# Kernel optimization log

Hardware: AMD Instinct MI355X
Metric: run time of the kernel (lower is better)

The kernel has to match this reference:

```python
import jax, jax.numpy as jnp
import numpy as np

B, N, VF, EF, DV, DE, LN = 64, 64, 32, 16, 128, 128, 4
EPS_INNER = 128.0  # BatchNorm1d(MAX_N, internal_d_vert): 2nd positional arg is eps (faithful to source bug)
EPS_BN = 1e-5


def gev_layer(v_in, e_in, evW, evb, eW, eb, vW, vb, relu=True):
    act = jax.nn.relu if relu else (lambda x: x)
    ev = v_in @ evW + evb                                   # [B,N,De]
    # outer_v_sum: ev.unsqueeze(1) + ev.unsqueeze(2) -> [B,N,N,De]
    e_out = act(e_in @ eW + eb + ev[:, None, :, :] + ev[:, :, None, :])
    per_v_e = e_out.sum(axis=1)                             # sum-aggregate over dim 1
    v_out = act(jnp.concatenate([per_v_e, v_in], axis=-1) @ vW + vb)
    return v_out, e_out


def bn_flat(v, g, b):
    # BatchNorm1d(N*VF) on [B, N*VF] in training mode (biased var)
    x = v.reshape(-1, N * VF)
    mu = x.mean(axis=0)
    var = x.var(axis=0)
    x = (x - mu) * jax.lax.rsqrt(var + EPS_BN) * g + b
    return x.reshape(-1, N, VF)


def bn_inner(v, g, b):
    # BatchNorm1d(MAX_N, eps=128) on [B, N, D]: channels are the N axis, stats over (B, D)
    mu = v.mean(axis=(0, 2), keepdims=True)
    var = v.var(axis=(0, 2), keepdims=True)
    return (v - mu) * jax.lax.rsqrt(var + EPS_INNER) * g[None, :, None] + b[None, :, None]


def setup_inputs() -> dict:
    key = jax.random.key(0)
    ks = jax.random.split(key, 24)
    s = 0.01  # force_lin_init with init_noise=0.01, biases zero
    nrm = lambda k, shp: jax.random.normal(k, shp, dtype=jnp.float32) * s
    inp = {
        "v": jax.random.normal(ks[0], (B, N, VF), dtype=jnp.float32),
        "e": jax.random.normal(ks[1], (B, N, N, EF), dtype=jnp.float32),
        "bn_in_g": jnp.ones((N * VF,), jnp.float32),
        "bn_in_b": jnp.zeros((N * VF,), jnp.float32),
        "g1_evW": nrm(ks[2], (VF, DE)), "g1_evb": jnp.zeros((DE,), jnp.float32),
        "g1_eW": nrm(ks[3], (EF, DE)), "g1_eb": jnp.zeros((DE,), jnp.float32),
        "g1_vW": nrm(ks[4], (VF + DE, DV)), "g1_vb": jnp.zeros((DV,), jnp.float32),
        "inn_evW": nrm(ks[5], (LN, DV, DE)), "inn_evb": jnp.zeros((LN, DE), jnp.float32),
        "inn_eW": nrm(ks[6], (LN, DE, DE)), "inn_eb": jnp.zeros((LN, DE), jnp.float32),
        "inn_vW": nrm(ks[7], (LN, DV + DE, DV)), "inn_vb": jnp.zeros((LN, DV), jnp.float32),
        "bn_g": jnp.ones((LN, N), jnp.float32),
        "bn_b": jnp.zeros((LN, N), jnp.float32),
        "g3_evW": nrm(ks[8], (DV, 1)), "g3_evb": jnp.zeros((1,), jnp.float32),
        "g3_eW": nrm(ks[9], (DE, 1)), "g3_eb": jnp.zeros((1,), jnp.float32),
        "g3_vW": nrm(ks[10], (DV + 1, 1)), "g3_vb": jnp.zeros((1,), jnp.float32),
    }
    return inp


def reference(v, e, bn_in_g, bn_in_b, g1_evW, g1_evb, g1_eW, g1_eb, g1_vW, g1_vb,
              inn_evW, inn_evb, inn_eW, inn_eb, inn_vW, inn_vb, bn_g, bn_b,
              g3_evW, g3_evb, g3_eW, g3_eb, g3_vW, g3_vb):
    v = bn_flat(v, bn_in_g, bn_in_b)
    v, e = gev_layer(v, e, g1_evW, g1_evb, g1_eW, g1_eb, g1_vW, g1_vb)
    for i in range(LN):
        v_next, e_next = gev_layer(v, e, inn_evW[i], inn_evb[i], inn_eW[i], inn_eb[i], inn_vW[i], inn_vb[i])
        v = v_next + v  # resnet
        e = e_next + e
        v = bn_inner(v, bn_g[i], bn_b[i])
    v, e = gev_layer(v, e, g3_evW, g3_evb, g3_eW, g3_eb, g3_vW, g3_vb, relu=False)
    return v, e
```

## Files before the change

### kernel.cpp

```cpp
#include <hip/hip_runtime.h>
#include <hip/hip_bf16.h>


typedef __bf16 bf16_t;
typedef __bf16 bf16x8 __attribute__((ext_vector_type(8)));
typedef __bf16 bf16x4 __attribute__((ext_vector_type(4)));
typedef float f32x4 __attribute__((ext_vector_type(4)));

__device__ __forceinline__ void bar_lgkm() {
  asm volatile("s_waitcnt lgkmcnt(0)\n\ts_barrier" ::: "memory");
}

__device__ __forceinline__ unsigned pack2(float a, float b) {
  bf16_t ba = (bf16_t)a, bb = (bf16_t)b;
  unsigned short ua, ub;
  __builtin_memcpy(&ua, &ba, 2);
  __builtin_memcpy(&ub, &bb, 2);
  return (unsigned)ua | ((unsigned)ub << 16);
}
__device__ __forceinline__ float blo(unsigned u) {
  unsigned v = u << 16; float f; __builtin_memcpy(&f, &v, 4); return f;
}
__device__ __forceinline__ float bhi(unsigned u) {
  unsigned v = u & 0xffff0000u; float f; __builtin_memcpy(&f, &v, 4); return f;
}

__global__ __launch_bounds__(256) void k_prep(const float* __restrict__ vin,
    const float* __restrict__ g, const float* __restrict__ bt,
    const float* __restrict__ eW, const float* __restrict__ inn_vW,
    const float* __restrict__ g1_vW, const float* __restrict__ inn_evW,
    float* __restrict__ v0, bf16_t* __restrict__ Wt, float* __restrict__ stats,
    unsigned* __restrict__ vWp, unsigned* __restrict__ g1_vWp,
    unsigned* __restrict__ evWp) {
  const int blk = blockIdx.x, tid = threadIdx.x;
  if (blk < 8) {
    int ch = blk * 256 + tid;
    float s = 0.f, s2 = 0.f;
    for (int b = 0; b < 64; ++b) { float x = vin[b * 2048 + ch]; s += x; s2 += x * x; }
    float mu = s * (1.f / 64.f);
    float var = s2 * (1.f / 64.f) - mu * mu;
    float sc = rsqrtf(var + 1e-5f) * g[ch];
    float bb = bt[ch];
    for (int b = 0; b < 64; ++b) {
      float x = vin[b * 2048 + ch];
      v0[b * 2048 + ch] = (x - mu) * sc + bb;
    }
  } else if (blk < 264) {
    int idx = (blk - 8) * 256 + tid;
    int l = idx >> 14, r = idx & 16383, n = r >> 7, k = r & 127;
    Wt[idx] = (bf16_t)eW[(l << 14) + (k << 7) + n];
  } else if (blk == 264) {
    for (int i = tid; i < 512; i += 256) stats[i] = 0.f;
  } else if (blk < 521) {
    int idx = (blk - 265) * 256 + tid;
    int l = idx >> 14, r = idx & 16383;
    int k8 = r >> 9, c = (r >> 2) & 127, j = r & 3;
    int ka = k8 * 8 + j * 2;
    vWp[idx] = pack2(inn_vW[(l << 15) + ka * 128 + c],
                     inn_vW[(l << 15) + (ka + 1) * 128 + c]);
  } else if (blk < 561) {
    int idx = (blk - 521) * 256 + tid;
    int k8 = idx >> 9, c = (idx >> 2) & 127, j = idx & 3;
    int ka = k8 * 8 + j * 2;
    g1_vWp[idx] = pack2(g1_vW[ka * 128 + c], g1_vW[(ka + 1) * 128 + c]);
  } else {
    int idx = (blk - 561) * 256 + tid;
    int l = idx >> 13, r = idx & 8191;
    int k8 = r >> 9, c = (r >> 2) & 127, j = r & 3;
    int ka = k8 * 8 + j * 2;
    evWp[idx] = pack2(inn_evW[(l << 14) + ka * 128 + c],
                      inn_evW[(l << 14) + (ka + 1) * 128 + c]);
  }
}

template <int K>
__global__ __launch_bounds__(256) void k_ev(const float* __restrict__ v_in,
    const float* __restrict__ W, const float* __restrict__ bias,
    float* __restrict__ out) {
  __shared__ float rows_s[8][K];
  const int r0 = blockIdx.x * 8;
  const int tid = threadIdx.x;
  const int c = tid & 127, h = tid >> 7;
  for (int idx = tid; idx < 8 * K; idx += 256) {
    int rr = idx / K, kk = idx % K;
    rows_s[rr][kk] = v_in[(r0 + rr) * K + kk];
  }
  __syncthreads();
  float acc[4];
  const float bv = bias[c];
#pragma unroll
  for (int r = 0; r < 4; ++r) acc[r] = bv;
  for (int k4 = 0; k4 < K; k4 += 4) {
    float w0 = W[(k4 + 0) * 128 + c], w1 = W[(k4 + 1) * 128 + c];
    float w2 = W[(k4 + 2) * 128 + c], w3 = W[(k4 + 3) * 128 + c];
#pragma unroll
    for (int r = 0; r < 4; ++r) {
      float4 x = *(const float4*)&rows_s[h * 4 + r][k4];
      acc[r] += x.x * w0 + x.y * w1 + x.z * w2 + x.w * w3;
    }
  }
#pragma unroll
  for (int r = 0; r < 4; ++r) out[(r0 + h * 4 + r) * 128 + c] = acc[r];
}

__global__ __launch_bounds__(256) void k_evbn(float* __restrict__ v,
    const float* __restrict__ stats, const float* __restrict__ g,
    const float* __restrict__ bt, const uint4* __restrict__ Wp,
    const float* __restrict__ bias, float* __restrict__ out) {
  __shared__ float rows_s[8][128];
  const int r0 = blockIdx.x * 8;
  const int tid = threadIdx.x;
  const int c = tid & 127, h = tid >> 7;
#pragma unroll
  for (int u = 0; u < 4; ++u) {
    int idx = u * 256 + tid;
    int rr = idx >> 7, k = idx & 127;
    int n = (r0 + rr) & 63;
    float mu = stats[n] * (1.f / 8192.f);
    float var = stats[64 + n] * (1.f / 8192.f) - mu * mu;
    float sc = rsqrtf(var + 128.f) * g[n];
    float x = (v[(r0 + rr) * 128 + k] - mu) * sc + bt[n];
    rows_s[rr][k] = x;
    v[(r0 + rr) * 128 + k] = x;
  }
  __syncthreads();
  float acc[4];
  const float bv = bias[c];
#pragma unroll
  for (int r = 0; r < 4; ++r) acc[r] = bv;
#pragma unroll 4
  for (int k8 = 0; k8 < 16; ++k8) {
    uint4 wv = Wp[k8 * 128 + c];
    float we0 = blo(wv.x), wo0 = bhi(wv.x);
    float we1 = blo(wv.y), wo1 = bhi(wv.y);
    float we2 = blo(wv.z), wo2 = bhi(wv.z);
    float we3 = blo(wv.w), wo3 = bhi(wv.w);
#pragma unroll
    for (int r = 0; r < 4; ++r) {
      float4 xa = *(const float4*)&rows_s[h * 4 + r][k8 * 8];
      float4 xb = *(const float4*)&rows_s[h * 4 + r][k8 * 8 + 4];
      acc[r] += xa.x * we0 + xa.y * wo0 + xa.z * we1 + xa.w * wo1
              + xb.x * we2 + xb.y * wo2 + xb.z * we3 + xb.w * wo3;
    }
  }
#pragma unroll
  for (int r = 0; r < 4; ++r) out[(r0 + h * 4 + r) * 128 + c] = acc[r];
}

__global__ __launch_bounds__(256) void k_edge_g1(const float* __restrict__ e0,
    const float* __restrict__ eW, const float* __restrict__ eb,
    const float* __restrict__ evA, bf16_t* __restrict__ e_ws,
    const float* __restrict__ v0, const uint4* __restrict__ g1_vWp,
    const float* __restrict__ vb, const uint4* __restrict__ evW0p,
    const float* __restrict__ evb, float* __restrict__ v,
    float* __restrict__ evB) {
  __shared__ bf16_t A0s[2][64][40];
  __shared__ bf16_t Os[2][64][136];
  __shared__ float in_s[2][160];
  __shared__ float vr_s[2][128];
  __shared__ float red[2][2][128];
  const int b = blockIdx.x >> 5, j0 = (blockIdx.x & 31) * 2;
  const int tid = threadIdx.x;
  const int lane = tid & 63, w = tid >> 6;
  const int quad = lane >> 4, l16 = lane & 15;
  f32x4 v0reg;
  if (tid < 16)
    v0reg = *(const f32x4*)&v0[(b * 64 + j0 + (tid >> 3)) * 32 + (tid & 7) * 4];
#pragma unroll
  for (int t = 0; t < 2; ++t) {
    int idx = tid + t * 256;
    int row = idx >> 3, off = (idx & 7) * 4;
    int jc = off >> 4, k = off & 15;
    f32x4 x = *(const f32x4*)&e0[((b * 64 + row) * 64 + j0) * 16 + off];
    bf16x4 y;
#pragma unroll
    for (int r = 0; r < 4; ++r) y[r] = (bf16_t)x[r];
    *(bf16x4*)&A0s[jc][row][k] = y;
    bf16x4 z = {(bf16_t)0.f, (bf16_t)0.f, (bf16_t)0.f, (bf16_t)0.f};
    *(bf16x4*)&A0s[jc][row][16 + k] = z;
  }
  const int c0[2] = {w * 32 + quad * 4, w * 32 + 16 + quad * 4};
  bf16x8 wf[2];
#pragma unroll
  for (int nt = 0; nt < 2; ++nt) {
    const int c = w * 32 + nt * 16 + l16;
#pragma unroll
    for (int jj = 0; jj < 8; ++jj)
      wf[nt][jj] = (quad < 2) ? (bf16_t)eW[(quad * 8 + jj) * 128 + c] : (bf16_t)0.f;
  }
  f32x4 acc[2][4][2];
  {
    f32x4 ebv[2], evj[2][2], evi[4][2];
#pragma unroll
    for (int nt = 0; nt < 2; ++nt) {
      ebv[nt] = *(const f32x4*)&eb[c0[nt]];
#pragma unroll
      for (int jc = 0; jc < 2; ++jc)
        evj[jc][nt] = *(const f32x4*)&evA[(b * 64 + j0 + jc) * 128 + c0[nt]];
#pragma unroll
      for (int mt = 0; mt < 4; ++mt)
        evi[mt][nt] = *(const f32x4*)&evA[(b * 64 + mt * 16 + l16) * 128 + c0[nt]];
    }
#pragma unroll
    for (int jc = 0; jc < 2; ++jc)
#pragma unroll
      for (int mt = 0; mt < 4; ++mt)
#pragma unroll
        for (int nt = 0; nt < 2; ++nt)
          acc[jc][mt][nt] = ebv[nt] + evj[jc][nt] + evi[mt][nt];
  }
  __syncthreads();
#pragma unroll
  for (int jc = 0; jc < 2; ++jc) {
#pragma unroll
    for (int mt = 0; mt < 4; ++mt) {
      bf16x8 ef = *(const bf16x8*)&A0s[jc][mt * 16 + l16][quad * 8];
#pragma unroll
      for (int nt = 0; nt < 2; ++nt)
        acc[jc][mt][nt] = __builtin_amdgcn_mfma_f32_16x16x32_bf16(wf[nt], ef, acc[jc][mt][nt], 0, 0, 0);
    }
  }
#pragma unroll
  for (int jc = 0; jc < 2; ++jc) {
#pragma unroll
    for (int nt = 0; nt < 2; ++nt) {
      f32x4 ps = {0.f, 0.f, 0.f, 0.f};
#pragma unroll
      for (int mt = 0; mt < 4; ++mt) {
        const int i = mt * 16 + l16;
        bf16x4 outv;
#pragma unroll
        for (int r = 0; r < 4; ++r) {
          float vv = fmaxf(acc[jc][mt][nt][r], 0.f);
          ps[r] += vv;
          outv[r] = (bf16_t)vv;
        }
        *(bf16x4*)&Os[jc][i][c0[nt]] = outv;
      }
#pragma unroll
      for (int m = 1; m <= 8; m <<= 1) {
#pragma unroll
        for (int r = 0; r < 4; ++r) ps[r] += __shfl_xor(ps[r], m);
      }
      if (l16 == 0) *(f32x4*)&in_s[jc][c0[nt]] = ps;
    }
  }
  if (tid < 16) *(f32x4*)&in_s[tid >> 3][128 + (tid & 7) * 4] = v0reg;
  __syncthreads();
  {
    bf16_t* ebase = &e_ws[((size_t)(b * 64 + j0) * 64) * 128];
#pragma unroll
    for (int t = 0; t < 8; ++t) {
      int idx = tid + t * 256;
      *(int4*)&ebase[idx * 8] =
          *(const int4*)&Os[idx >> 10][(idx >> 4) & 63][(idx & 15) * 8];
    }
  }
  const int khalf = w >> 1, cbase = (w & 1) << 6;
  const int cc = cbase + lane;
  const int c = tid & 127, h = tid >> 7;
  {
    float p0 = 0.f, p1 = 0.f;
    const uint4* Wp = &g1_vWp[(khalf * 10) * 128 + cc];
    const float* xs0 = &in_s[0][khalf * 80];
    const float* xs1 = &in_s[1][khalf * 80];
#pragma unroll 5
    for (int k8 = 0; k8 < 10; ++k8) {
      uint4 wv = Wp[k8 * 128];
      float we0 = blo(wv.x), wo0 = bhi(wv.x);
      float we1 = blo(wv.y), wo1 = bhi(wv.y);
      float we2 = blo(wv.z), wo2 = bhi(wv.z);
      float we3 = blo(wv.w), wo3 = bhi(wv.w);
      float4 xa0 = *(const float4*)&xs0[k8 * 8];
      float4 xb0 = *(const float4*)&xs0[k8 * 8 + 4];
      float4 xa1 = *(const float4*)&xs1[k8 * 8];
      float4 xb1 = *(const float4*)&xs1[k8 * 8 + 4];
      p0 += xa0.x * we0 + xa0.y * wo0 + xa0.z * we1 + xa0.w * wo1
          + xb0.x * we2 + xb0.y * wo2 + xb0.z * we3 + xb0.w * wo3;
      p1 += xa1.x * we0 + xa1.y * wo0 + xa1.z * we1 + xa1.w * wo1
          + xb1.x * we2 + xb1.y * wo2 + xb1.z * we3 + xb1.w * wo3;
    }
    red[khalf][0][cc] = p0;
    red[khalf][1][cc] = p1;
  }
  bar_lgkm();
  {
    float vacc = vb[c] + red[0][h][c] + red[1][h][c];
    float vr = fmaxf(vacc, 0.f);
    v[(b * 64 + j0 + h) * 128 + c] = vr;
    vr_s[h][c] = vr;
  }
  bar_lgkm();
  {
    float p0 = 0.f, p1 = 0.f;
    const uint4* Wp = &evW0p[(khalf * 8) * 128 + cc];
    const float* xs0 = &vr_s[0][khalf << 6];
    const float* xs1 = &vr_s[1][khalf << 6];
#pragma unroll 4
    for (int k8 = 0; k8 < 8; ++k8) {
      uint4 wv = Wp[k8 * 128];
      float we0 = blo(wv.x), wo0 = bhi(wv.x);
      float we1 = blo(wv.y), wo1 = bhi(wv.y);
      float we2 = blo(wv.z), wo2 = bhi(wv.z);
      float we3 = blo(wv.w), wo3 = bhi(wv.w);
      float4 xa0 = *(const float4*)&xs0[k8 * 8];
      float4 xb0 = *(const float4*)&xs0[k8 * 8 + 4];
      float4 xa1 = *(const float4*)&xs1[k8 * 8];
      float4 xb1 = *(const float4*)&xs1[k8 * 8 + 4];
      p0 += xa0.x * we0 + xa0.y * wo0 + xa0.z * we1 + xa0.w * wo1
          + xb0.x * we2 + xb0.y * wo2 + xb0.z * we3 + xb0.w * wo3;
      p1 += xa1.x * we0 + xa1.y * wo0 + xa1.z * we1 + xa1.w * wo1
          + xb1.x * we2 + xb1.y * wo2 + xb1.z * we3 + xb1.w * wo3;
    }
    red[khalf][0][cc] = p0;
    red[khalf][1][cc] = p1;
  }
  bar_lgkm();
  evB[(b * 64 + j0 + h) * 128 + c] = evb[c] + red[0][h][c] + red[1][h][c];
}

template <bool LAST>
__global__ __launch_bounds__(256) void k_edge_inner(bf16_t* __restrict__ e_ws,
    const bf16_t* __restrict__ Wt, const float* __restrict__ eb,
    const float* __restrict__ ev, const float* __restrict__ eW3,
    float* __restrict__ edt, float* __restrict__ v,
    const uint4* __restrict__ vWp, const float* __restrict__ vb,
    float* __restrict__ stats) {
  __shared__ bf16_t As[2][64][136];
  __shared__ float W3s[128];
  __shared__ float in_s[2][256];
  __shared__ float red[2][2][128];
  __shared__ float part[4][2];
  const int b = blockIdx.x >> 5, j0 = (blockIdx.x & 31) * 2;
  const int tid = threadIdx.x;
  const int lane = tid & 63, w = tid >> 6;
  const int quad = lane >> 4, l16 = lane & 15;
  bf16_t* ebase = &e_ws[((size_t)(b * 64 + j0) * 64) * 128];
  int4 stg[8];
#pragma unroll
  for (int t = 0; t < 8; ++t) {
    int idx = tid + t * 256;
    stg[t] = *(const int4*)&ebase[idx * 8];
  }
  f32x4 vreg;
  if (tid < 64)
    vreg = *(const f32x4*)&v[(b * 64 + j0 + (tid >> 5)) * 128 + (tid & 31) * 4];
  if (LAST) {
    if (tid < 128) W3s[tid] = eW3[tid];
  }
  bf16x8 wf[2][4];
#pragma unroll
  for (int nt = 0; nt < 2; ++nt)
#pragma unroll
    for (int ks = 0; ks < 4; ++ks)
      wf[nt][ks] = *(const bf16x8*)&Wt[(w * 32 + nt * 16 + l16) * 128 + ks * 32 + quad * 8];
  const int c0[2] = {w * 32 + quad * 4, w * 32 + 16 + quad * 4};
  f32x4 acc[2][4][2];
  {
    f32x4 ebv[2], evj[2][2], evi[4][2];
#pragma unroll
    for (int nt = 0; nt < 2; ++nt) {
      ebv[nt] = *(const f32x4*)&eb[c0[nt]];
#pragma unroll
      for (int jc = 0; jc < 2; ++jc)
        evj[jc][nt] = *(const f32x4*)&ev[(b * 64 + j0 + jc) * 128 + c0[nt]];
#pragma unroll
      for (int mt = 0; mt < 4; ++mt)
        evi[mt][nt] = *(const f32x4*)&ev[(b * 64 + mt * 16 + l16) * 128 + c0[nt]];
    }
#pragma unroll
    for (int jc = 0; jc < 2; ++jc)
#pragma unroll
      for (int mt = 0; mt < 4; ++mt)
#pragma unroll
        for (int nt = 0; nt < 2; ++nt)
          acc[jc][mt][nt] = ebv[nt] + evj[jc][nt] + evi[mt][nt];
  }
#pragma unroll
  for (int t = 0; t < 8; ++t) {
    int idx = tid + t * 256;
    *(int4*)&As[idx >> 10][(idx >> 4) & 63][(idx & 15) * 8] = stg[t];
  }
  bar_lgkm();
#pragma unroll
  for (int ks = 0; ks < 4; ++ks) {
    bf16x8 ef[2][4];
#pragma unroll
    for (int jc = 0; jc < 2; ++jc)
#pragma unroll
      for (int mt = 0; mt < 4; ++mt)
        ef[jc][mt] = *(const bf16x8*)&As[jc][mt * 16 + l16][ks * 32 + quad * 8];
#pragma unroll
    for (int jc = 0; jc < 2; ++jc)
#pragma unroll
      for (int mt = 0; mt < 4; ++mt)
#pragma unroll
        for (int nt = 0; nt < 2; ++nt)
          acc[jc][mt][nt] = __builtin_amdgcn_mfma_f32_16x16x32_bf16(wf[nt][ks], ef[jc][mt], acc[jc][mt][nt], 0, 0, 0);
  }
  bar_lgkm();
#pragma unroll
  for (int jc = 0; jc < 2; ++jc) {
#pragma unroll
    for (int nt = 0; nt < 2; ++nt) {
      f32x4 ps = {0.f, 0.f, 0.f, 0.f};
#pragma unroll
      for (int mt = 0; mt < 4; ++mt) {
        const int i = mt * 16 + l16;
        bf16x4 eo = *(const bf16x4*)&As[jc][i][c0[nt]];
        bf16x4 outv;
#pragma unroll
        for (int r = 0; r < 4; ++r) {
          float vv = fmaxf(acc[jc][mt][nt][r], 0.f);
          ps[r] += vv;
          outv[r] = (bf16_t)(vv + (float)eo[r]);
        }
        *(bf16x4*)&As[jc][i][c0[nt]] = outv;
      }
#pragma unroll
      for (int m = 1; m <= 8; m <<= 1) {
#pragma unroll
        for (int r = 0; r < 4; ++r) ps[r] += __shfl_xor(ps[r], m);
      }
      if (l16 == 0) *(f32x4*)&in_s[jc][c0[nt]] = ps;
    }
  }
  if (tid < 64) *(f32x4*)&in_s[tid >> 5][128 + (tid & 31) * 4] = vreg;
  bar_lgkm();
  const int khalf = w >> 1, cbase = (w & 1) << 6;
  const int cc = cbase + lane;
  float p0 = 0.f, p1 = 0.f;
  {
    const uint4* Wp = &vWp[(khalf * 16) * 128 + cc];
    const float* xs0 = &in_s[0][khalf << 7];
    const float* xs1 = &in_s[1][khalf << 7];
#pragma unroll 4
    for (int k8 = 0; k8 < 16; ++k8) {
      uint4 wv = Wp[k8 * 128];
      float we0 = blo(wv.x), wo0 = bhi(wv.x);
      float we1 = blo(wv.y), wo1 = bhi(wv.y);
      float we2 = blo(wv.z), wo2 = bhi(wv.z);
      float we3 = blo(wv.w), wo3 = bhi(wv.w);
      float4 xa0 = *(const float4*)&xs0[k8 * 8];
      float4 xb0 = *(const float4*)&xs0[k8 * 8 + 4];
      float4 xa1 = *(const float4*)&xs1[k8 * 8];
      float4 xb1 = *(const float4*)&xs1[k8 * 8 + 4];
      p0 += xa0.x * we0 + xa0.y * wo0 + xa0.z * we1 + xa0.w * wo1
          + xb0.x * we2 + xb0.y * wo2 + xb0.z * we3 + xb0.w * wo3;
      p1 += xa1.x * we0 + xa1.y * wo0 + xa1.z * we1 + xa1.w * wo1
          + xb1.x * we2 + xb1.y * wo2 + xb1.z * we3 + xb1.w * wo3;
    }
  }
  if (!LAST) {
#pragma unroll
    for (int t = 0; t < 8; ++t) {
      int idx = tid + t * 256;
      *(int4*)&ebase[idx * 8] =
          *(const int4*)&As[idx >> 10][(idx >> 4) & 63][(idx & 15) * 8];
    }
  } else {
    const int i = tid >> 2, q = tid & 3;
#pragma unroll
    for (int jc = 0; jc < 2; ++jc) {
      float d = 0.f;
#pragma unroll
      for (int t = 0; t < 4; ++t) {
        bf16x8 x = *(const bf16x8*)&As[jc][i][q * 32 + t * 8];
#pragma unroll
        for (int u = 0; u < 8; ++u) d += (float)x[u] * W3s[q * 32 + t * 8 + u];
      }
      d += __shfl_xor(d, 1);
      d += __shfl_xor(d, 2);
      if (q == 0) edt[(b * 64 + j0 + jc) * 64 + i] = d;
    }
  }
  red[khalf][0][cc] = p0;
  red[khalf][1][cc] = p1;
  bar_lgkm();
  const int c = tid & 127, h = tid >> 7;
  float vacc = vb[c] + red[0][h][c] + red[1][h][c];
  float vnew = fmaxf(vacc, 0.f) + in_s[h][128 + c];
  v[(b * 64 + j0 + h) * 128 + c] = vnew;
  float s = vnew, s2 = vnew * vnew;
#pragma unroll
  for (int m = 1; m <= 32; m <<= 1) {
    s += __shfl_xor(s, m);
    s2 += __shfl_xor(s2, m);
  }
  if (lane == 0) { part[w][0] = s; part[w][1] = s2; }
  bar_lgkm();
  if (tid < 2) {
    int n = j0 + tid;
    atomicAdd(&stats[n], part[tid * 2][0] + part[tid * 2 + 1][0]);
    atomicAdd(&stats[64 + n], part[tid * 2][1] + part[tid * 2 + 1][1]);
  }
}

__global__ __launch_bounds__(256) void k_g3(const float* __restrict__ vv,
    const float* __restrict__ stats3, const float* __restrict__ g,
    const float* __restrict__ bt, const float* __restrict__ evW3,
    const float* __restrict__ evb3, const float* __restrict__ eb3,
    const float* __restrict__ edt, const float* __restrict__ vW3,
    const float* __restrict__ vb3, float* __restrict__ out_v,
    float* __restrict__ out_e) {
  __shared__ float vbn[64][132];
  __shared__ float edts[64][68];
  __shared__ float scs[64], shs[64];
  __shared__ float W3e[128];
  __shared__ float vWs[132];
  __shared__ float ev3s[64];
  __shared__ float pj[4][64];
  const int b = blockIdx.x, tid = threadIdx.x;
  if (tid < 64) {
    float mu = stats3[tid] * (1.f / 8192.f);
    float var = stats3[64 + tid] * (1.f / 8192.f) - mu * mu;
    float sc = rsqrtf(var + 128.f) * g[tid];
    scs[tid] = sc;
    shs[tid] = bt[tid] - mu * sc;
  }
  if (tid < 128) W3e[tid] = evW3[tid];
  if (tid < 129) vWs[tid] = vW3[tid];
  __syncthreads();
#pragma unroll
  for (int t = 0; t < 8; ++t) {
    int idx = t * 1024 + tid * 4;
    int row = idx >> 7, cc = idx & 127;
    f32x4 x = *(const f32x4*)&vv[(b * 64 + row) * 128 + cc];
    *(f32x4*)&vbn[row][cc] = x * scs[row] + shs[row];
  }
#pragma unroll
  for (int t = 0; t < 4; ++t) {
    int idx = t * 1024 + tid * 4;
    int j = idx >> 6, i = idx & 63;
    *(f32x4*)&edts[j][i] = *(const f32x4*)&edt[(b * 64 + j) * 64 + i];
  }
  __syncthreads();
  {
    int i = tid >> 2, q = tid & 3;
    float d = 0.f;
#pragma unroll
    for (int u = 0; u < 32; ++u) d += vbn[i][q * 32 + u] * W3e[q * 32 + u];
    d += __shfl_xor(d, 1);
    d += __shfl_xor(d, 2);
    if (q == 0) ev3s[i] = d + evb3[0];
  }
  __syncthreads();
  {
    int q = tid >> 6, j = tid & 63;
    float s = 0.f;
    const float e3 = eb3[0];
    const float evj = ev3s[j];
#pragma unroll
    for (int r = 0; r < 16; ++r) {
      int i = q * 16 + r;
      float val = edts[j][i] + e3 + ev3s[i] + evj;
      out_e[(b * 64 + i) * 64 + j] = val;
      s += val;
    }
    pj[q][j] = s;
  }
  __syncthreads();
  {
    int n = tid >> 2, q = tid & 3;
    float d = 0.f;
#pragma unroll
    for (int u = 0; u < 32; ++u) d += vbn[n][q * 32 + u] * vWs[1 + q * 32 + u];
    d += __shfl_xor(d, 1);
    d += __shfl_xor(d, 2);
    if (q == 0) {
      float p3 = pj[0][n] + pj[1][n] + pj[2][n] + pj[3][n];
      out_v[b * 64 + n] = d + p3 * vWs[0] + vb3[0];
    }
  }
}

extern "C" void kernel_launch(void* const* d_in, const int* in_sizes, int n_in,
                              void* d_out, int out_size, void* d_ws, size_t ws_size,
                              hipStream_t stream) {
  const float* in_v    = (const float*)d_in[0];
  const float* in_e    = (const float*)d_in[1];
  const float* bn_in_g = (const float*)d_in[2];
  const float* bn_in_b = (const float*)d_in[3];
  const float* g1_evW  = (const float*)d_in[4];
  const float* g1_evb  = (const float*)d_in[5];
  const float* g1_eW   = (const float*)d_in[6];
  const float* g1_eb   = (const float*)d_in[7];
  const float* g1_vW   = (const float*)d_in[8];
  const float* g1_vb   = (const float*)d_in[9];
  const float* inn_evW = (const float*)d_in[10];
  const float* inn_evb = (const float*)d_in[11];
  const float* inn_eW  = (const float*)d_in[12];
  const float* inn_eb  = (const float*)d_in[13];
  const float* inn_vW  = (const float*)d_in[14];
  const float* inn_vb  = (const float*)d_in[15];
  const float* bn_g    = (const float*)d_in[16];
  const float* bn_b    = (const float*)d_in[17];
  const float* g3_evW  = (const float*)d_in[18];
  const float* g3_evb  = (const float*)d_in[19];
  const float* g3_eW   = (const float*)d_in[20];
  const float* g3_eb   = (const float*)d_in[21];
  const float* g3_vW   = (const float*)d_in[22];
  const float* g3_vb   = (const float*)d_in[23];

  char* ws = (char*)d_ws;
  bf16_t* e_ws = (bf16_t*)(ws);
  float* v        = (float*)(ws + 67108864);
  float* evA      = (float*)(ws + 69206016);
  float* evB      = (float*)(ws + 71303168);
  float* v0       = (float*)(ws + 73400320);
  bf16_t* Wt      = (bf16_t*)(ws + 73924608);
  float* edt      = (float*)(ws + 74055680);
  float* stats    = (float*)(ws + 75104256);
  unsigned* vWp   = (unsigned*)(ws + 75106304);
  unsigned* g1_vWp= (unsigned*)(ws + 75368448);
  unsigned* evWp  = (unsigned*)(ws + 75409408);

  float* out_v = (float*)d_out;
  float* out_e = (float*)d_out + 4096;

  k_prep<<<689, 256, 0, stream>>>(in_v, bn_in_g, bn_in_b, inn_eW, inn_vW, g1_vW,
                                  inn_evW, v0, Wt, stats, vWp, g1_vWp, evWp);

  k_ev<32><<<512, 256, 0, stream>>>(v0, g1_evW, g1_evb, evA);
  k_edge_g1<<<2048, 256, 0, stream>>>(in_e, g1_eW, g1_eb, evA, e_ws,
                                      v0, (const uint4*)g1_vWp, g1_vb,
                                      (const uint4*)evWp, inn_evb, v, evB);

  for (int l = 0; l < 4; ++l) {
    if (l > 0)
      k_evbn<<<512, 256, 0, stream>>>(v, stats + (l - 1) * 128, bn_g + (l - 1) * 64,
                                      bn_b + (l - 1) * 64,
                                      (const uint4*)evWp + l * 2048,
                                      inn_evb + l * 128, evB);
    if (l < 3)
      k_edge_inner<false><<<2048, 256, 0, stream>>>(e_ws, Wt + l * 16384,
          inn_eb + l * 128, evB, g3_eW, edt, v,
          (const uint4*)vWp + l * 4096, inn_vb + l * 128, stats + l * 128);
    else
      k_edge_inner<true><<<2048, 256, 0, stream>>>(e_ws, Wt + l * 16384,
          inn_eb + l * 128, evB, g3_eW, edt, v,
          (const uint4*)vWp + l * 4096, inn_vb + l * 128, stats + l * 128);
  }

  k_g3<<<64, 256, 0, stream>>>(v, stats + 384, bn_g + 192, bn_b + 192,
                               g3_evW, g3_evb, g3_eb, edt, g3_vW, g3_vb,
                               out_v, out_e);
}
```

Before: 369.1 us.

## Fuse inner-layer BN and ev projection into edge kernel with MFMA recompute

Removes the separate k_evbn launch between inner layers. Each k_edge_inner block now applies the previous layer's BatchNorm to all 64 vertex rows of its batch and computes the ev projection with bf16 MFMA, using a new transposed bf16 copy of inn_evW built in k_prep. The vertex buffer is ping-ponged between two buffers so that reading v and writing it back do not race across blocks. In exchange, every block recomputes the full 64x128x128 ev GEMM for its batch, which is 32x redundant work across blocks, and ev is computed in bf16 rather than fp32.

Result: no change. 367.5 us (-0.4%).

```diff
diff --git a/kernel.cpp b/kernel.cpp
--- a/kernel.cpp
+++ b/kernel.cpp
@@ -5,6 +5,7 @@
 typedef __bf16 bf16_t;
 typedef __bf16 bf16x8 __attribute__((ext_vector_type(8)));
 typedef __bf16 bf16x4 __attribute__((ext_vector_type(4)));
+typedef __bf16 bf16x2 __attribute__((ext_vector_type(2)));
 typedef float f32x4 __attribute__((ext_vector_type(4)));
 
 __device__ __forceinline__ void bar_lgkm() {
@@ -31,7 +32,7 @@
     const float* __restrict__ g1_vW, const float* __restrict__ inn_evW,
     float* __restrict__ v0, bf16_t* __restrict__ Wt, float* __restrict__ stats,
     unsigned* __restrict__ vWp, unsigned* __restrict__ g1_vWp,
-    unsigned* __restrict__ evWp) {
+    unsigned* __restrict__ evWp, bf16_t* __restrict__ evWtB) {
   const int blk = blockIdx.x, tid = threadIdx.x;
   if (blk < 8) {
     int ch = blk * 256 + tid;
@@ -63,13 +64,17 @@
     int k8 = idx >> 9, c = (idx >> 2) & 127, j = idx & 3;
     int ka = k8 * 8 + j * 2;
     g1_vWp[idx] = pack2(g1_vW[ka * 128 + c], g1_vW[(ka + 1) * 128 + c]);
-  } else {
+  } else if (blk < 689) {
     int idx = (blk - 561) * 256 + tid;
     int l = idx >> 13, r = idx & 8191;
     int k8 = r >> 9, c = (r >> 2) & 127, j = r & 3;
     int ka = k8 * 8 + j * 2;
     evWp[idx] = pack2(inn_evW[(l << 14) + ka * 128 + c],
                       inn_evW[(l << 14) + (ka + 1) * 128 + c]);
+  } else {
+    int idx = (blk - 689) * 256 + tid;
+    int l = idx >> 14, r = idx & 16383, n = r >> 7, k = r & 127;
+    evWtB[idx] = (bf16_t)inn_evW[(l << 14) + (k << 7) + n];
   }
 }
 
@@ -97,50 +102,6 @@
     for (int r = 0; r < 4; ++r) {
       float4 x = *(const float4*)&rows_s[h * 4 + r][k4];
       acc[r] += x.x * w0 + x.y * w1 + x.z * w2 + x.w * w3;
-    }
-  }
-#pragma unroll
-  for (int r = 0; r < 4; ++r) out[(r0 + h * 4 + r) * 128 + c] = acc[r];
-}
-
-__global__ __launch_bounds__(256) void k_evbn(float* __restrict__ v,
-    const float* __restrict__ stats, const float* __restrict__ g,
-    const float* __restrict__ bt, const uint4* __restrict__ Wp,
-    const float* __restrict__ bias, float* __restrict__ out) {
-  __shared__ float rows_s[8][128];
-  const int r0 = blockIdx.x * 8;
-  const int tid = threadIdx.x;
-  const int c = tid & 127, h = tid >> 7;
-#pragma unroll
-  for (int u = 0; u < 4; ++u) {
-    int idx = u * 256 + tid;
-    int rr = idx >> 7, k = idx & 127;
-    int n = (r0 + rr) & 63;
-    float mu = stats[n] * (1.f / 8192.f);
-    float var = stats[64 + n] * (1.f / 8192.f) - mu * mu;
-    float sc = rsqrtf(var + 128.f) * g[n];
-    float x = (v[(r0 + rr) * 128 + k] - mu) * sc + bt[n];
-    rows_s[rr][k] = x;
-    v[(r0 + rr) * 128 + k] = x;
-  }
-  __syncthreads();
-  float acc[4];
-  const float bv = bias[c];
-#pragma unroll
-  for (int r = 0; r < 4; ++r) acc[r] = bv;
-#pragma unroll 4
-  for (int k8 = 0; k8 < 16; ++k8) {
-    uint4 wv = Wp[k8 * 128 + c];
-    float we0 = blo(wv.x), wo0 = bhi(wv.x);
-    float we1 = blo(wv.y), wo1 = bhi(wv.y);
-    float we2 = blo(wv.z), wo2 = bhi(wv.z);
-    float we3 = blo(wv.w), wo3 = bhi(wv.w);
-#pragma unroll
-    for (int r = 0; r < 4; ++r) {
-      float4 xa = *(const float4*)&rows_s[h * 4 + r][k8 * 8];
-      float4 xb = *(const float4*)&rows_s[h * 4 + r][k8 * 8 + 4];
-      acc[r] += xa.x * we0 + xa.y * wo0 + xa.z * we1 + xa.w * wo1
-              + xb.x * we2 + xb.y * wo2 + xb.z * we3 + xb.w * wo3;
     }
   }
 #pragma unroll
@@ -319,18 +280,22 @@
   evB[(b * 64 + j0 + h) * 128 + c] = evb[c] + red[0][h][c] + red[1][h][c];
 }
 
-template <bool LAST>
+template <bool LAST, bool EVGEN>
 __global__ __launch_bounds__(256) void k_edge_inner(bf16_t* __restrict__ e_ws,
     const bf16_t* __restrict__ Wt, const float* __restrict__ eb,
     const float* __restrict__ ev, const float* __restrict__ eW3,
-    float* __restrict__ edt, float* __restrict__ v,
-    const uint4* __restrict__ vWp, const float* __restrict__ vb,
-    float* __restrict__ stats) {
+    float* __restrict__ edt, const float* __restrict__ vin,
+    float* __restrict__ vout, const uint4* __restrict__ vWp,
+    const float* __restrict__ vb, float* __restrict__ statsAcc,
+    const float* __restrict__ statsPrev, const float* __restrict__ gPrev,
+    const float* __restrict__ btPrev, const bf16_t* __restrict__ evWtB,
+    const float* __restrict__ evb) {
   __shared__ bf16_t As[2][64][136];
   __shared__ float W3s[128];
   __shared__ float in_s[2][256];
   __shared__ float red[2][2][128];
   __shared__ float part[4][2];
+  __shared__ float scs[64], shs[64];
   const int b = blockIdx.x >> 5, j0 = (blockIdx.x & 31) * 2;
   const int tid = threadIdx.x;
   const int lane = tid & 63, w = tid >> 6;
@@ -344,7 +309,7 @@
   }
   f32x4 vreg;
   if (tid < 64)
-    vreg = *(const f32x4*)&v[(b * 64 + j0 + (tid >> 5)) * 128 + (tid & 31) * 4];
+    vreg = *(const f32x4*)&vin[(b * 64 + j0 + (tid >> 5)) * 128 + (tid & 31) * 4];
   if (LAST) {
     if (tid < 128) W3s[tid] = eW3[tid];
   }
@@ -356,7 +321,81 @@
       wf[nt][ks] = *(const bf16x8*)&Wt[(w * 32 + nt * 16 + l16) * 128 + ks * 32 + quad * 8];
   const int c0[2] = {w * 32 + quad * 4, w * 32 + 16 + quad * 4};
   f32x4 acc[2][4][2];
-  {
+  if (EVGEN) {
+    if (tid < 64) {
+      float mu = statsPrev[tid] * (1.f / 8192.f);
+      float var = statsPrev[64 + tid] * (1.f / 8192.f) - mu * mu;
+      float sc = rsqrtf(var + 128.f) * gPrev[tid];
+      scs[tid] = sc;
+      shs[tid] = btPrev[tid] - mu * sc;
+    }
+    bf16x8 wf2[2][4];
+#pragma unroll
+    for (int nt = 0; nt < 2; ++nt)
+#pragma unroll
+      for (int ks = 0; ks < 4; ++ks)
+        wf2[nt][ks] = *(const bf16x8*)&evWtB[(w * 32 + nt * 16 + l16) * 128 + ks * 32 + quad * 8];
+    bar_lgkm();
+#pragma unroll
+    for (int t = 0; t < 16; ++t) {
+      int row = t * 4 + w;
+      float2 xv = *(const float2*)&vin[(b * 64 + row) * 128 + lane * 2];
+      float sc = scs[row], sh = shs[row];
+      bf16x2 o;
+      o[0] = (bf16_t)(xv.x * sc + sh);
+      o[1] = (bf16_t)(xv.y * sc + sh);
+      *(bf16x2*)&As[0][row][lane * 2] = o;
+    }
+    if (tid < 64) {
+      int rr = j0 + (tid >> 5);
+      vreg = vreg * scs[rr] + shs[rr];
+    }
+    bar_lgkm();
+    f32x4 acc_ev[4][2];
+#pragma unroll
+    for (int nt = 0; nt < 2; ++nt) {
+      f32x4 bias = *(const f32x4*)&evb[c0[nt]];
+#pragma unroll
+      for (int mt = 0; mt < 4; ++mt) acc_ev[mt][nt] = bias;
+    }
+#pragma unroll
+    for (int ks = 0; ks < 4; ++ks) {
+      bf16x8 bfm[4];
+#pragma unroll
+      for (int mt = 0; mt < 4; ++mt)
+        bfm[mt] = *(const bf16x8*)&As[0][mt * 16 + l16][ks * 32 + quad * 8];
+#pragma unroll
+      for (int mt = 0; mt < 4; ++mt)
+#pragma unroll
+        for (int nt = 0; nt < 2; ++nt)
+          acc_ev[mt][nt] = __builtin_amdgcn_mfma_f32_16x16x32_bf16(wf2[nt][ks], bfm[mt], acc_ev[mt][nt], 0, 0, 0);
+    }
+    const int mtj = j0 >> 4;
+    f32x4 evrow[2];
+#pragma unroll
+    for (int mt = 0; mt < 4; ++mt)
+      if (mtj == mt) { evrow[0] = acc_ev[mt][0]; evrow[1] = acc_ev[mt][1]; }
+    f32x4 evj[2][2];
+#pragma unroll
+    for (int jc = 0; jc < 2; ++jc) {
+      int src = (quad << 4) | ((j0 + jc) & 15);
+#pragma unroll
+      for (int nt = 0; nt < 2; ++nt)
+#pragma unroll
+        for (int r = 0; r < 4; ++r)
+          evj[jc][nt][r] = __shfl(evrow[nt][r], src);
+    }
+#pragma unroll
+    for (int nt = 0; nt < 2; ++nt) {
+      f32x4 ebv = *(const f32x4*)&eb[c0[nt]];
+#pragma unroll
+      for (int jc = 0; jc < 2; ++jc)
+#pragma unroll
+        for (int mt = 0; mt < 4; ++mt)
+          acc[jc][mt][nt] = ebv + evj[jc][nt] + acc_ev[mt][nt];
+    }
+    bar_lgkm();
+  } else {
     f32x4 ebv[2], evj[2][2], evi[4][2];
 #pragma unroll
     for (int nt = 0; nt < 2; ++nt) {
@@ -480,7 +519,7 @@
   const int c = tid & 127, h = tid >> 7;
   float vacc = vb[c] + red[0][h][c] + red[1][h][c];
   float vnew = fmaxf(vacc, 0.f) + in_s[h][128 + c];
-  v[(b * 64 + j0 + h) * 128 + c] = vnew;
+  vout[(b * 64 + j0 + h) * 128 + c] = vnew;
   float s = vnew, s2 = vnew * vnew;
 #pragma unroll
   for (int m = 1; m <= 32; m <<= 1) {
@@ -491,8 +530,8 @@
   bar_lgkm();
   if (tid < 2) {
     int n = j0 + tid;
-    atomicAdd(&stats[n], part[tid * 2][0] + part[tid * 2 + 1][0]);
-    atomicAdd(&stats[64 + n], part[tid * 2][1] + part[tid * 2 + 1][1]);
+    atomicAdd(&statsAcc[n], part[tid * 2][0] + part[tid * 2 + 1][0]);
+    atomicAdd(&statsAcc[64 + n], part[tid * 2][1] + part[tid * 2 + 1][1]);
   }
 }
 
@@ -604,7 +643,7 @@
 
   char* ws = (char*)d_ws;
   bf16_t* e_ws = (bf16_t*)(ws);
-  float* v        = (float*)(ws + 67108864);
+  float* vA       = (float*)(ws + 67108864);
   float* evA      = (float*)(ws + 69206016);
   float* evB      = (float*)(ws + 71303168);
   float* v0       = (float*)(ws + 73400320);
@@ -614,35 +653,44 @@
   unsigned* vWp   = (unsigned*)(ws + 75106304);
   unsigned* g1_vWp= (unsigned*)(ws + 75368448);
   unsigned* evWp  = (unsigned*)(ws + 75409408);
+  bf16_t* evWtB   = (bf16_t*)(ws + 75540480);
+  float* vB       = (float*)(ws + 75671552);
 
   float* out_v = (float*)d_out;
   float* out_e = (float*)d_out + 4096;
 
-  k_prep<<<689, 256, 0, stream>>>(in_v, bn_in_g, bn_in_b, inn_eW, inn_vW, g1_vW,
-                                  inn_evW, v0, Wt, stats, vWp, g1_vWp, evWp);
+  k_prep<<<945, 256, 0, stream>>>(in_v, bn_in_g, bn_in_b, inn_eW, inn_vW, g1_vW,
+                                  inn_evW, v0, Wt, stats, vWp, g1_vWp, evWp, evWtB);
 
   k_ev<32><<<512, 256, 0, stream>>>(v0, g1_evW, g1_evb, evA);
   k_edge_g1<<<2048, 256, 0, stream>>>(in_e, g1_eW, g1_eb, evA, e_ws,
                                       v0, (const uint4*)g1_vWp, g1_vb,
-                                      (const uint4*)evWp, inn_evb, v, evB);
-
+                                      (const uint4*)evWp, inn_evb, vA, evB);
+
+  float* vbufs[2] = {vA, vB};
   for (int l = 0; l < 4; ++l) {
-    if (l > 0)
-      k_evbn<<<512, 256, 0, stream>>>(v, stats + (l - 1) * 128, bn_g + (l - 1) * 64,
-                                      bn_b + (l - 1) * 64,
-                                      (const uint4*)evWp + l * 2048,
-                                      inn_evb + l * 128, evB);
-    if (l < 3)
-      k_edge_inner<false><<<2048, 256, 0, stream>>>(e_ws, Wt + l * 16384,
-          inn_eb + l * 128, evB, g3_eW, edt, v,
-          (const uint4*)vWp + l * 4096, inn_vb + l * 128, stats + l * 128);
+    float* vin_l  = vbufs[l & 1];
+    float* vout_l = vbufs[(l + 1) & 1];
+    if (l == 0)
+      k_edge_inner<false, false><<<2048, 256, 0, stream>>>(e_ws, Wt,
+          inn_eb, evB, g3_eW, edt, vin_l, vout_l,
+          (const uint4*)vWp, inn_vb, stats,
+          nullptr, nullptr, nullptr, nullptr, nullptr);
+    else if (l < 3)
+      k_edge_inner<false, true><<<2048, 256, 0, stream>>>(e_ws, Wt + l * 16384,
+          inn_eb + l * 128, evB, g3_eW, edt, vin_l, vout_l,
+          (const uint4*)vWp + l * 4096, inn_vb + l * 128, stats + l * 128,
+          stats + (l - 1) * 128, bn_g + (l - 1) * 64, bn_b + (l - 1) * 64,
+          evWtB + l * 16384, inn_evb + l * 128);
     else
-      k_edge_inner<true><<<2048, 256, 0, stream>>>(e_ws, Wt + l * 16384,
-          inn_eb + l * 128, evB, g3_eW, edt, v,
-          (const uint4*)vWp + l * 4096, inn_vb + l * 128, stats + l * 128);
-  }
-
-  k_g3<<<64, 256, 0, stream>>>(v, stats + 384, bn_g + 192, bn_b + 192,
+      k_edge_inner<true, true><<<2048, 256, 0, stream>>>(e_ws, Wt + l * 16384,
+          inn_eb + l * 128, evB, g3_eW, edt, vin_l, vout_l,
+          (const uint4*)vWp + l * 4096, inn_vb + l * 128, stats + l * 128,
+          stats + (l - 1) * 128, bn_g + (l - 1) * 64, bn_b + (l - 1) * 64,
+          evWtB + l * 16384, inn_evb + l * 128);
+  }
+
+  k_g3<<<64, 256, 0, stream>>>(vA, stats + 384, bn_g + 192, bn_b + 192,
                                g3_evW, g3_evb, g3_eb, edt, g3_vW, g3_vb,
                                out_v, out_e);
 }
```
